# Kernel tuning notes

Hardware: AMD Instinct MI355X
Metric: run time of the kernel (lower is better)

## Reference

```python
import jax, jax.numpy as jnp
import numpy as np

C = 1024
FACTOR = 4
C_INT = C * FACTOR


def setup_inputs() -> dict:
    key = jax.random.key(0)
    ks = jax.random.split(key, 6)
    act = jax.random.normal(ks[0], (4, 2048, C), dtype=jnp.float32)
    mask = jnp.ones((4, 2048), dtype=jnp.float32)
    # LayerNorm params
    ln_scale = jnp.ones((C,), dtype=jnp.float32)
    ln_bias = jnp.zeros((C,), dtype=jnp.float32)
    # Linear 1 (init='linear'): lecun-normal-ish
    w1 = jax.random.normal(ks[1], (C, C_INT), dtype=jnp.float32) / np.sqrt(C)
    b1 = jnp.zeros((C_INT,), dtype=jnp.float32)
    # Linear 2 (init='final' -> zeros in AF2; use small random so grads are nontrivial)
    w2 = jax.random.normal(ks[2], (C_INT, C), dtype=jnp.float32) * 0.02
    b2 = jnp.zeros((C,), dtype=jnp.float32)
    return {"act": act, "mask": mask, "ln_scale": ln_scale, "ln_bias": ln_bias,
            "w1": w1, "b1": b1, "w2": w2, "b2": b2}


def _layernorm(x, scale, bias, eps=1e-5):
    mu = jnp.mean(x, axis=-1, keepdims=True)
    var = jnp.mean(jnp.square(x - mu), axis=-1, keepdims=True)
    return (x - mu) * jax.lax.rsqrt(var + eps) * scale + bias


def reference(act, mask, ln_scale, ln_bias, w1, b1, w2, b2):
    # mask is accepted but unused, matching the original forward.
    x = _layernorm(act, ln_scale, ln_bias)
    h = jax.nn.relu(jnp.einsum('bsc,cf->bsf', x, w1) + b1)
    return jnp.einsum('bsf,fc->bsc', h, w2) + b2
```

## Files before the change

kernel.cpp:

```cpp
#include <hip/hip_runtime.h>
#include <hip/hip_bf16.h>
#include <cstdint>

typedef unsigned short u16;
typedef __bf16 bf16x8 __attribute__((ext_vector_type(8)));
typedef float floatx4 __attribute__((ext_vector_type(4)));

#define AS1 __attribute__((address_space(1)))
#define AS3 __attribute__((address_space(3)))

static __device__ __forceinline__ u16 f2bf(float f) {
    union { float f; unsigned int u; } v; v.f = f;
    unsigned int u = v.u;
    return (u16)((u + 0x7FFFu + ((u >> 16) & 1u)) >> 16);
}

__device__ __forceinline__ void transpose_body(
    const float* __restrict__ in, u16* __restrict__ out,
    int R, int Ccols, int bx, int by, int tid, float (*tile)[33])
{
    const int tx = tid & 31;
    const int ty = tid >> 5;
    const int c0 = bx * 32;
    const int r0 = by * 32;
#pragma unroll
    for (int i = 0; i < 32; i += 8)
        tile[ty + i][tx] = in[(size_t)(r0 + ty + i) * Ccols + (c0 + tx)];
    __syncthreads();
#pragma unroll
    for (int i = 0; i < 32; i += 8)
        out[(size_t)(c0 + ty + i) * R + (r0 + tx)] = f2bf(tile[tx][ty + i]);
}

__global__ __launch_bounds__(256)
void prep(const float* __restrict__ w1, const float* __restrict__ w2,
          const float* __restrict__ act, const float* __restrict__ ln_scale,
          const float* __restrict__ ln_bias,
          u16* __restrict__ W1t, u16* __restrict__ W2t, u16* __restrict__ X)
{
    __shared__ float smem[32][33];
    const int id  = blockIdx.x;
    const int tid = threadIdx.x;

    if (id < 4096) {
        transpose_body(w1, W1t, 1024, 4096, id & 127, id >> 7, tid, smem);
        return;
    }
    if (id < 8192) {
        const int t = id - 4096;
        transpose_body(w2, W2t, 4096, 1024, t & 31, t >> 5, tid, smem);
        return;
    }
    const int row = id - 8192;
    const float4 v = ((const float4*)(act + (size_t)row * 1024))[tid];
    float s  = v.x + v.y + v.z + v.w;
    float ss = v.x * v.x + v.y * v.y + v.z * v.z + v.w * v.w;
#pragma unroll
    for (int off = 32; off > 0; off >>= 1) {
        s  += __shfl_xor(s, off, 64);
        ss += __shfl_xor(ss, off, 64);
    }
    float* red = &smem[0][0];
    const int wave = tid >> 6, lane = tid & 63;
    if (lane == 0) { red[wave] = s; red[4 + wave] = ss; }
    __syncthreads();
    s  = red[0] + red[1] + red[2] + red[3];
    ss = red[4] + red[5] + red[6] + red[7];
    const float mu  = s * (1.0f / 1024.0f);
    const float var = ss * (1.0f / 1024.0f) - mu * mu;
    const float rs  = rsqrtf(var + 1e-5f);
    const float4 sc = ((const float4*)ln_scale)[tid];
    const float4 bi = ((const float4*)ln_bias)[tid];
    ushort4 o;
    o.x = f2bf((v.x - mu) * rs * sc.x + bi.x);
    o.y = f2bf((v.y - mu) * rs * sc.y + bi.y);
    o.z = f2bf((v.z - mu) * rs * sc.z + bi.z);
    o.w = f2bf((v.w - mu) * rs * sc.w + bi.w);
    ((ushort4*)(X + (size_t)row * 1024))[tid] = o;
}

template <int BK, bool BF16_OUT, bool RELU>
__global__ __launch_bounds__(256)
void gemm_bt(const u16* __restrict__ A,
             const u16* __restrict__ Bt,
             const float* __restrict__ bias,
             void* __restrict__ Cout,
             int M, int N, int K)
{
    constexpr int SLOTS  = BK / 8;
    constexpr int RPI    = 64 / SLOTS;
    constexpr int IPW    = SLOTS / 2;
    constexpr int HALVES = BK / 32;

    __shared__ __align__(16) u16 Alds[128 * BK];
    __shared__ __align__(16) u16 Blds[128 * BK];

    const int tid  = threadIdx.x;
    const int wave = tid >> 6;
    const int lane = tid & 63;
    const int wm   = wave & 1;
    const int wn   = wave >> 1;
    const int quad = lane >> 4;
    const int l16  = lane & 15;

    const int nbm = M >> 7;
    const int id  = blockIdx.x;
    const int bm  = id % nbm;
    const int bn  = id / nbm;

    const u16* Ag = A  + (size_t)bm * 128 * K;
    const u16* Bg = Bt + (size_t)bn * 128 * K;

    const int srow = lane / SLOTS;
    const int s_st = lane & (SLOTS - 1);

    const int rkey = (SLOTS == 4) ? ((l16 >> 1) & 3) : (l16 & (SLOTS - 1));

    floatx4 acc[4][4];
#pragma unroll
    for (int i = 0; i < 4; ++i)
#pragma unroll
        for (int j = 0; j < 4; ++j)
            acc[i][j] = (floatx4){0.f, 0.f, 0.f, 0.f};

    for (int k0 = 0; k0 < K; k0 += BK) {
        __syncthreads();
#pragma unroll
        for (int r = 0; r < IPW; ++r) {
            const int chunk = wave * IPW + r;
            const int row = chunk * RPI + srow;
            const int key = (SLOTS == 4) ? ((row >> 1) & 3)
                                         : (row & (SLOTS - 1));
            const int scol = (s_st ^ key) * 8;
            __builtin_amdgcn_global_load_lds(
                (AS1 void*)(Ag + (size_t)row * K + k0 + scol),
                (AS3 void*)(&Alds[chunk * 512]), 16, 0, 0);
            __builtin_amdgcn_global_load_lds(
                (AS1 void*)(Bg + (size_t)row * K + k0 + scol),
                (AS3 void*)(&Blds[chunk * 512]), 16, 0, 0);
        }
        __syncthreads();

#pragma unroll
        for (int h = 0; h < HALVES; ++h) {
            const int slot = ((quad + 4 * h) ^ rkey) * 8;
            bf16x8 bfr[4];
#pragma unroll
            for (int ni = 0; ni < 4; ++ni) {
                const int brow = wn * 64 + ni * 16 + l16;
                bfr[ni] = *(const bf16x8*)(&Blds[brow * BK + slot]);
            }
#pragma unroll
            for (int mi = 0; mi < 4; ++mi) {
                const int arow = wm * 64 + mi * 16 + l16;
                const bf16x8 a = *(const bf16x8*)(&Alds[arow * BK + slot]);
#pragma unroll
                for (int ni = 0; ni < 4; ++ni)
                    acc[mi][ni] = __builtin_amdgcn_mfma_f32_16x16x32_bf16(
                        bfr[ni], a, acc[mi][ni], 0, 0, 0);
            }
        }
    }

    const int mbase = bm * 128 + wm * 64;
    const int nbase = bn * 128 + wn * 64;
#pragma unroll
    for (int mi = 0; mi < 4; ++mi) {
        const int m = mbase + mi * 16 + l16;
#pragma unroll
        for (int ni = 0; ni < 4; ++ni) {
            const int n0 = nbase + ni * 16 + quad * 4;
            const float4 bv = *(const float4*)&bias[n0];
            float v0 = acc[mi][ni][0] + bv.x;
            float v1 = acc[mi][ni][1] + bv.y;
            float v2 = acc[mi][ni][2] + bv.z;
            float v3 = acc[mi][ni][3] + bv.w;
            if (RELU) {
                v0 = fmaxf(v0, 0.f); v1 = fmaxf(v1, 0.f);
                v2 = fmaxf(v2, 0.f); v3 = fmaxf(v3, 0.f);
            }
            if (BF16_OUT) {
                ushort4 o = { f2bf(v0), f2bf(v1), f2bf(v2), f2bf(v3) };
                *(ushort4*)&((u16*)Cout)[(size_t)m * N + n0] = o;
            } else {
                float4 o = { v0, v1, v2, v3 };
                *(float4*)&((float*)Cout)[(size_t)m * N + n0] = o;
            }
        }
    }
}

extern "C" void kernel_launch(void* const* d_in, const int* in_sizes, int n_in,
                              void* d_out, int out_size, void* d_ws, size_t ws_size,
                              hipStream_t stream)
{
    const float* act      = (const float*)d_in[0];
    const float* ln_scale = (const float*)d_in[2];
    const float* ln_bias  = (const float*)d_in[3];
    const float* w1       = (const float*)d_in[4];
    const float* b1       = (const float*)d_in[5];
    const float* w2       = (const float*)d_in[6];
    const float* b2       = (const float*)d_in[7];
    float* out = (float*)d_out;

    const int M = 8192, C = 1024, CI = 4096;

    u16* X   = (u16*)d_ws;
    u16* W1t = X   + (size_t)M * C;
    u16* W2t = W1t + (size_t)CI * C;
    u16* H   = W2t + (size_t)C * CI;

    prep<<<16384, 256, 0, stream>>>(w1, w2, act, ln_scale, ln_bias, W1t, W2t, X);
    gemm_bt<64, true, true><<<(M / 128) * (CI / 128), 256, 0, stream>>>(
        X, W1t, b1, (void*)H, M, CI, C);
    gemm_bt<128, false, false><<<(M / 128) * (C / 128), 256, 0, stream>>>(
        H, W2t, b2, (void*)out, M, C, CI);
}
```

Before: 266.9 us.

## Overlap W2 transpose with GEMM1 and prefetch next K tile during last MFMA half

Moves the W2 fp32-to-bf16 transpose out of the prep kernel into extra tail blocks of the first GEMM launch, so that work runs alongside GEMM1 instead of ahead of it. The GEMM main loop is also restructured: the final k-half's fragments are loaded into registers, then the next tile's global-to-LDS loads are issued before that half's MFMAs. This overlaps load latency with compute using a single buffer. The cost is an extra barrier per iteration, and the transpose blocks' shared tile may add LDS usage to the GEMM kernel, which could lower occupancy.

```diff
diff --git a/kernel.cpp b/kernel.cpp
--- a/kernel.cpp
+++ b/kernel.cpp
@@ -33,10 +33,9 @@
 }
 
 __global__ __launch_bounds__(256)
-void prep(const float* __restrict__ w1, const float* __restrict__ w2,
-          const float* __restrict__ act, const float* __restrict__ ln_scale,
-          const float* __restrict__ ln_bias,
-          u16* __restrict__ W1t, u16* __restrict__ W2t, u16* __restrict__ X)
+void prep(const float* __restrict__ w1, const float* __restrict__ act,
+          const float* __restrict__ ln_scale, const float* __restrict__ ln_bias,
+          u16* __restrict__ W1t, u16* __restrict__ X)
 {
     __shared__ float smem[32][33];
     const int id  = blockIdx.x;
@@ -46,12 +45,7 @@
         transpose_body(w1, W1t, 1024, 4096, id & 127, id >> 7, tid, smem);
         return;
     }
-    if (id < 8192) {
-        const int t = id - 4096;
-        transpose_body(w2, W2t, 4096, 1024, t & 31, t >> 5, tid, smem);
-        return;
-    }
-    const int row = id - 8192;
+    const int row = id - 4096;
     const float4 v = ((const float4*)(act + (size_t)row * 1024))[tid];
     float s  = v.x + v.y + v.z + v.w;
     float ss = v.x * v.x + v.y * v.y + v.z * v.z + v.w * v.w;
@@ -79,18 +73,36 @@
     ((ushort4*)(X + (size_t)row * 1024))[tid] = o;
 }
 
-template <int BK, bool BF16_OUT, bool RELU>
+template <int BK, bool BF16_OUT, bool RELU, bool TRANS>
 __global__ __launch_bounds__(256)
 void gemm_bt(const u16* __restrict__ A,
              const u16* __restrict__ Bt,
              const float* __restrict__ bias,
              void* __restrict__ Cout,
-             int M, int N, int K)
+             int M, int N, int K,
+             const float* __restrict__ tin,
+             u16* __restrict__ tout,
+             int TR, int TC)
 {
     constexpr int SLOTS  = BK / 8;
     constexpr int RPI    = 64 / SLOTS;
     constexpr int IPW    = SLOTS / 2;
     constexpr int HALVES = BK / 32;
+
+    const int nbm = M >> 7;
+    const int nbn = N >> 7;
+    const int id  = blockIdx.x;
+
+    if constexpr (TRANS) {
+        if (id >= nbm * nbn) {
+            __shared__ float tile[32][33];
+            const int t   = id - nbm * nbn;
+            const int nbx = TC / 32;
+            transpose_body(tin, tout, TR, TC, t % nbx, t / nbx,
+                           threadIdx.x, tile);
+            return;
+        }
+    }
 
     __shared__ __align__(16) u16 Alds[128 * BK];
     __shared__ __align__(16) u16 Blds[128 * BK];
@@ -103,8 +115,6 @@
     const int quad = lane >> 4;
     const int l16  = lane & 15;
 
-    const int nbm = M >> 7;
-    const int id  = blockIdx.x;
     const int bm  = id % nbm;
     const int bn  = id / nbm;
 
@@ -113,18 +123,9 @@
 
     const int srow = lane / SLOTS;
     const int s_st = lane & (SLOTS - 1);
-
     const int rkey = (SLOTS == 4) ? ((l16 >> 1) & 3) : (l16 & (SLOTS - 1));
 
-    floatx4 acc[4][4];
-#pragma unroll
-    for (int i = 0; i < 4; ++i)
-#pragma unroll
-        for (int j = 0; j < 4; ++j)
-            acc[i][j] = (floatx4){0.f, 0.f, 0.f, 0.f};
-
-    for (int k0 = 0; k0 < K; k0 += BK) {
-        __syncthreads();
+    auto stage = [&](int k0) {
 #pragma unroll
         for (int r = 0; r < IPW; ++r) {
             const int chunk = wave * IPW + r;
@@ -139,10 +140,21 @@
                 (AS1 void*)(Bg + (size_t)row * K + k0 + scol),
                 (AS3 void*)(&Blds[chunk * 512]), 16, 0, 0);
         }
-        __syncthreads();
-
-#pragma unroll
-        for (int h = 0; h < HALVES; ++h) {
+    };
+
+    floatx4 acc[4][4];
+#pragma unroll
+    for (int i = 0; i < 4; ++i)
+#pragma unroll
+        for (int j = 0; j < 4; ++j)
+            acc[i][j] = (floatx4){0.f, 0.f, 0.f, 0.f};
+
+    stage(0);
+    __syncthreads();
+
+    for (int k0 = 0; k0 < K; k0 += BK) {
+#pragma unroll
+        for (int h = 0; h < HALVES - 1; ++h) {
             const int slot = ((quad + 4 * h) ^ rkey) * 8;
             bf16x8 bfr[4];
 #pragma unroll
@@ -160,6 +172,27 @@
                         bfr[ni], a, acc[mi][ni], 0, 0, 0);
             }
         }
+        const int slotL = ((quad + 4 * (HALVES - 1)) ^ rkey) * 8;
+        bf16x8 aL[4], bL[4];
+#pragma unroll
+        for (int mi = 0; mi < 4; ++mi) {
+            const int arow = wm * 64 + mi * 16 + l16;
+            aL[mi] = *(const bf16x8*)(&Alds[arow * BK + slotL]);
+        }
+#pragma unroll
+        for (int ni = 0; ni < 4; ++ni) {
+            const int brow = wn * 64 + ni * 16 + l16;
+            bL[ni] = *(const bf16x8*)(&Blds[brow * BK + slotL]);
+        }
+        __syncthreads();
+        if (k0 + BK < K) stage(k0 + BK);
+#pragma unroll
+        for (int mi = 0; mi < 4; ++mi)
+#pragma unroll
+            for (int ni = 0; ni < 4; ++ni)
+                acc[mi][ni] = __builtin_amdgcn_mfma_f32_16x16x32_bf16(
+                    bL[ni], aL[mi], acc[mi][ni], 0, 0, 0);
+        __syncthreads();
     }
 
     const int mbase = bm * 128 + wm * 64;
@@ -210,9 +243,11 @@
     u16* W2t = W1t + (size_t)CI * C;
     u16* H   = W2t + (size_t)C * CI;
 
-    prep<<<16384, 256, 0, stream>>>(w1, w2, act, ln_scale, ln_bias, W1t, W2t, X);
-    gemm_bt<64, true, true><<<(M / 128) * (CI / 128), 256, 0, stream>>>(
-        X, W1t, b1, (void*)H, M, CI, C);
-    gemm_bt<128, false, false><<<(M / 128) * (C / 128), 256, 0, stream>>>(
-        H, W2t, b2, (void*)out, M, C, CI);
-}
+    prep<<<12288, 256, 0, stream>>>(w1, act, ln_scale, ln_bias, W1t, X);
+    gemm_bt<64, true, true, true>
+        <<<(M / 128) * (CI / 128) + 4096, 256, 0, stream>>>(
+        X, W1t, b1, (void*)H, M, CI, C, w2, W2t, 4096, 1024);
+    gemm_bt<128, false, false, false>
+        <<<(M / 128) * (C / 128), 256, 0, stream>>>(
+        H, W2t, b2, (void*)out, M, C, CI, nullptr, nullptr, 0, 0);
+}
```

Result: slower. 277.5 us (+4.0%).
